# Optimization experiments

Measured on AMD Instinct MI355X. Metric: run time of the kernel, lower is better.

The kernel has to match this reference:

```python
import jax, jax.numpy as jnp
import numpy as np

T, B, OBS, LS, H, NA = 256, 1024, 128, 128, 128, 18


def setup_inputs() -> dict:
    key = jax.random.key(0)
    ks = jax.random.split(key, 20)
    rn = lambda i, shape, sc: jax.random.normal(ks[i], shape, dtype=jnp.float32) * sc
    return {
        "x": jax.random.normal(ks[0], (T * B, OBS), dtype=jnp.float32),
        "done": (jax.random.uniform(ks[1], (T * B,)) < 0.05).astype(jnp.float32),
        "h0": rn(2, (1, B, H), 0.1),
        "c0": rn(3, (1, B, H), 0.1),
        # MLP encoder: obs -> 128 -> 32 -> lstm_size
        "W1": rn(4, (128, OBS), 0.1), "b1": jnp.zeros((128,), jnp.float32),
        "W2": rn(5, (32, 128), 0.1), "b2": jnp.zeros((32,), jnp.float32),
        "W3": rn(6, (LS, 32), 0.1), "b3": jnp.zeros((LS,), jnp.float32),
        # LSTM params, PyTorch gate order [i, f, g, o]
        "Wih": rn(7, (4 * H, LS), 0.1), "Whh": rn(8, (4 * H, H), 0.1),
        "bih": jnp.zeros((4 * H,), jnp.float32), "bhh": jnp.zeros((4 * H,), jnp.float32),
        "Wa": rn(9, (NA, H), 0.01), "ba": jnp.zeros((NA,), jnp.float32),
        "Wc": rn(10, (1, H), 0.1), "bc": jnp.zeros((1,), jnp.float32),
    }


def reference(x, done, h0, c0, W1, b1, W2, b2, W3, b3, Wih, Whh, bih, bhh, Wa, ba, Wc, bc):
    # MLP encoder (self.network)
    hid = jax.nn.relu(x @ W1.T + b1)
    hid = jax.nn.relu(hid @ W2.T + b2)
    hid = jax.nn.relu(hid @ W3.T + b3)           # [T*B, LS]
    Bsz = h0.shape[1]
    hid = hid.reshape(-1, Bsz, hid.shape[-1])    # [T, B, LS]
    d = done.reshape(-1, Bsz)                    # [T, B]

    Hh = h0.shape[-1]

    def step(carry, inp):
        h, c = carry
        xt, dt = inp
        m = (1.0 - dt)[:, None]                  # reset mask
        h = h * m
        c = c * m
        gates = xt @ Wih.T + bih + h @ Whh.T + bhh   # [B, 4H]
        i = jax.nn.sigmoid(gates[:, :Hh])
        f = jax.nn.sigmoid(gates[:, Hh:2 * Hh])
        g = jnp.tanh(gates[:, 2 * Hh:3 * Hh])
        o = jax.nn.sigmoid(gates[:, 3 * Hh:])
        c = f * c + i * g
        h = o * jnp.tanh(c)
        return (h, c), h

    (hN, cN), hs = jax.lax.scan(step, (h0[0], c0[0]), (hid, d))
    flat = hs.reshape(-1, Hh)                    # [T*B, H]
    logits = flat @ Wa.T + ba                    # actor head
    value = flat @ Wc.T + bc                     # critic head
    return jnp.concatenate([logits, value], axis=-1)  # [T*B, NA+1]
```

## Files before the change

kernel.cpp:

```cpp
#include <hip/hip_runtime.h>
#include <hip/hip_bf16.h>

typedef unsigned short u16;
typedef unsigned int u32;
typedef __attribute__((ext_vector_type(8))) short short8;
typedef __attribute__((ext_vector_type(4))) float f4;
typedef __attribute__((ext_vector_type(4))) u32 u4;

#define MFMA(a, b, c) __builtin_amdgcn_mfma_f32_16x16x32_bf16((a), (b), (c), 0, 0, 0)

#define TT 256
#define BB 1024
#define NN (TT * BB)
#define NCHUNK (NN / 16)
#define WS_HID3 0
#define WS_WF   (NN * 128)
#define OFF_W1  0
#define OFF_W2  16384
#define OFF_W3  20480
#define OFF_WIH 24576
#define OFF_WHH 90112
#define OFF_WA  155648
#define WF_TOT  159744

static __device__ __forceinline__ u16 f2bf(float f) {
    u32 u = __float_as_uint(f);
    u32 r = (u + 0x7FFFu + ((u >> 16) & 1u)) >> 16;
    return (u16)r;
}
static __device__ __forceinline__ short8 pack8(f4 a, f4 b) {
    short8 r;
    r[0] = (short)f2bf(a[0]); r[1] = (short)f2bf(a[1]);
    r[2] = (short)f2bf(a[2]); r[3] = (short)f2bf(a[3]);
    r[4] = (short)f2bf(b[0]); r[5] = (short)f2bf(b[1]);
    r[6] = (short)f2bf(b[2]); r[7] = (short)f2bf(b[3]);
    return r;
}
static __device__ __forceinline__ short8 u4_to_s8(u4 v) {
    union { u4 u; short8 s; } t; t.u = v; return t.s;
}
static __device__ __forceinline__ float sigf(float x) {
    return __builtin_amdgcn_rcpf(1.f + __builtin_amdgcn_exp2f(-1.442695040888963f * x));
}
static __device__ __forceinline__ float tanhf_fast(float x) {
    return 2.f * __builtin_amdgcn_rcpf(1.f + __builtin_amdgcn_exp2f(-2.885390081777927f * x)) - 1.f;
}

static __device__ void convW128(const float* src, int Nn, u16* dst, int tid, int nth) {
    int tot = Nn * 128;
    for (int d = tid; d < tot; d += nth) {
        int j = d & 7, l = (d >> 3) & 63, ck = d >> 9;
        int kc = ck & 3, nt = ck >> 2;
        int n = nt * 16 + (l & 15), k = kc * 32 + ((l >> 4) << 3) + j;
        dst[d] = f2bf(src[n * 128 + k]);
    }
}
static __device__ void convW32(const float* src, int Nn, u16* dst, int tid, int nth) {
    int tot = Nn * 32;
    for (int d = tid; d < tot; d += nth) {
        int j = d & 7, l = (d >> 3) & 63, nt = d >> 9;
        int n = nt * 16 + (l & 15), k = ((l >> 4) << 3) + j;
        dst[d] = f2bf(src[n * 32 + k]);
    }
}

__global__ void k0_conv(const float* __restrict__ W1, const float* __restrict__ W2,
                        const float* __restrict__ W3, const float* __restrict__ Wih,
                        const float* __restrict__ Whh, const float* __restrict__ Wa,
                        const float* __restrict__ Wc, u16* __restrict__ wf) {
    int tid = blockIdx.x * blockDim.x + threadIdx.x;
    int nth = gridDim.x * blockDim.x;
    convW128(W1, 128, wf + OFF_W1, tid, nth);
    convW128(W2, 32, wf + OFF_W2, tid, nth);
    convW32(W3, 128, wf + OFF_W3, tid, nth);
    convW128(Wih, 512, wf + OFF_WIH, tid, nth);
    convW128(Whh, 512, wf + OFF_WHH, tid, nth);
    for (int d = tid; d < 32 * 128; d += nth) {
        int j = d & 7, l = (d >> 3) & 63, ck = d >> 9;
        int kc = ck & 3, nt = ck >> 2;
        int n = nt * 16 + (l & 15), k = kc * 32 + ((l >> 4) << 3) + j;
        float v = (n < 18) ? Wa[n * 128 + k] : ((n == 18) ? Wc[k] : 0.f);
        wf[OFF_WA + d] = f2bf(v);
    }
}

__global__ __launch_bounds__(256) void k1_enc(
    const float* __restrict__ x, const float* __restrict__ b1, const float* __restrict__ b2,
    const float* __restrict__ b3, const u16* __restrict__ wf, u16* __restrict__ hid3f) {
    __shared__ __align__(16) u16 scr[4][2560];

    int tid = threadIdx.x, wv = tid >> 6, lane = tid & 63;
    int m = lane & 15, q = lane >> 4;
    u16* s1 = scr[wv];
    u16* s2 = scr[wv] + 2048;
    const short8* W1v = (const short8*)(wf + OFF_W1);
    const short8* W2v = (const short8*)(wf + OFF_W2);
    const short8* W3v = (const short8*)(wf + OFF_W3);
    int wid = blockIdx.x * 4 + wv;

    for (int it = 0; it < 8; ++it) {
        int c = wid + it * 2048;
        short8 a1[4];
        const float* xr = x + (size_t)(c * 16 + m) * 128 + q * 8;
#pragma unroll
        for (int kc = 0; kc < 4; ++kc) {
            f4 f0 = *(const f4*)(xr + kc * 32);
            f4 f1 = *(const f4*)(xr + kc * 32 + 4);
            a1[kc] = pack8(f0, f1);
        }
#pragma unroll
        for (int nt = 0; nt < 8; ++nt) {
            f4 acc = {0.f, 0.f, 0.f, 0.f};
#pragma unroll
            for (int kc = 0; kc < 4; ++kc) acc = MFMA(a1[kc], W1v[(nt * 4 + kc) * 64 + lane], acc);
            int col = nt * 16 + m;
            float bb = b1[col];
            int base = (col >> 5) * 512 + ((col >> 3) & 3) * 128 + (col & 7);
#pragma unroll
            for (int p = 0; p < 4; ++p) {
                float v = acc[p] + bb; v = v > 0.f ? v : 0.f;
                s1[base + (q * 4 + p) * 8] = f2bf(v);
            }
        }
        __syncthreads();
        short8 a2[4];
#pragma unroll
        for (int kc = 0; kc < 4; ++kc) a2[kc] = *(const short8*)(s1 + kc * 512 + lane * 8);
#pragma unroll
        for (int nt = 0; nt < 2; ++nt) {
            f4 acc = {0.f, 0.f, 0.f, 0.f};
#pragma unroll
            for (int kc = 0; kc < 4; ++kc) acc = MFMA(a2[kc], W2v[(nt * 4 + kc) * 64 + lane], acc);
            int col = nt * 16 + m;
            float bb = b2[col];
            int base = (col >> 3) * 128 + (col & 7);
#pragma unroll
            for (int p = 0; p < 4; ++p) {
                float v = acc[p] + bb; v = v > 0.f ? v : 0.f;
                s2[base + (q * 4 + p) * 8] = f2bf(v);
            }
        }
        __syncthreads();
        short8 a3 = *(const short8*)(s2 + lane * 8);
#pragma unroll
        for (int nt = 0; nt < 8; ++nt) {
            f4 acc = {0.f, 0.f, 0.f, 0.f};
            acc = MFMA(a3, W3v[nt * 64 + lane], acc);
            int col = nt * 16 + m;
            float bb = b3[col];
            int base = (col >> 5) * 512 + ((col >> 3) & 3) * 128 + (col & 7);
#pragma unroll
            for (int p = 0; p < 4; ++p) {
                float v = acc[p] + bb; v = v > 0.f ? v : 0.f;
                s1[base + (q * 4 + p) * 8] = f2bf(v);
            }
        }
        __syncthreads();
        u4* dst = (u4*)hid3f + (size_t)c * 256;
#pragma unroll
        for (int kc = 0; kc < 4; ++kc) dst[kc * 64 + lane] = *(const u4*)(s1 + kc * 512 + lane * 8);
    }
}

__global__ __launch_bounds__(512) void k3_lstm(
    u16* __restrict__ hws,
    const u16* __restrict__ wf, const float* __restrict__ bih, const float* __restrict__ bhh,
    const float* __restrict__ done, const float* __restrict__ h0, const float* __restrict__ c0) {
    __shared__ __align__(16) u16 hbuf[2][2048];
    __shared__ __align__(16) float dls[4096];

    int tid = threadIdx.x, wv = tid >> 6, lane = tid & 63;
    int u15 = lane & 15, q = lane >> 4;
    int u = wv * 16 + u15;
    int rb = blockIdx.x * 16;
    const short8* WHv = (const short8*)(wf + OFF_WHH);
    const short8* WIv = (const short8*)(wf + OFF_WIH);

    short8 wh[4][4], wi[4][4];
#pragma unroll
    for (int g = 0; g < 4; ++g)
#pragma unroll
        for (int kc = 0; kc < 4; ++kc) {
            int nt = g * 8 + wv;
            wh[g][kc] = WHv[(nt * 4 + kc) * 64 + lane];
            wi[g][kc] = WIv[(nt * 4 + kc) * 64 + lane];
        }
    float bg[4];
#pragma unroll
    for (int g = 0; g < 4; ++g) bg[g] = bih[g * 128 + u] + bhh[g * 128 + u];

    for (int i = tid; i < 4096; i += 512) {
        int t = i >> 4, r = i & 15;
        dls[i] = 1.0f - done[(size_t)t * BB + rb + r];
    }
    float cst[4];
#pragma unroll
    for (int k = 0; k < 4; ++k) {
        int r = 4 * q + k;
        cst[k] = c0[(size_t)(rb + r) * 128 + u];
        float hv = h0[(size_t)(rb + r) * 128 + u];
        hbuf[0][(u >> 5) * 512 + (((u >> 3) & 3) * 16 + r) * 8 + (u & 7)] = f2bf(hv);
    }
    const u4* h3 = (const u4*)hws;
    u4 xf[4];
#pragma unroll
    for (int kc = 0; kc < 4; ++kc)
        xf[kc] = h3[((size_t)blockIdx.x * 4 + kc) * 64 + lane];
    __syncthreads();

    for (int t = 0; t < TT; ++t) {
        const u16* hc = hbuf[t & 1];
        u16* hn = hbuf[(t + 1) & 1];
        short8 ah[4];
#pragma unroll
        for (int kc = 0; kc < 4; ++kc) ah[kc] = *(const short8*)(hc + kc * 512 + lane * 8);
        f4 aH[4], aX[4];
#pragma unroll
        for (int g = 0; g < 4; ++g) { aH[g] = (f4){0.f, 0.f, 0.f, 0.f}; aX[g] = (f4){0.f, 0.f, 0.f, 0.f}; }
#pragma unroll
        for (int kc = 0; kc < 4; ++kc) {
            short8 xs = u4_to_s8(xf[kc]);
#pragma unroll
            for (int g = 0; g < 4; ++g) {
                aH[g] = MFMA(ah[kc], wh[g][kc], aH[g]);
                aX[g] = MFMA(xs, wi[g][kc], aX[g]);
            }
        }
        if (t < TT - 1) {
#pragma unroll
            for (int kc = 0; kc < 4; ++kc)
                xf[kc] = h3[(((size_t)(t + 1) * 64 + blockIdx.x) * 4 + kc) * 64 + lane];
        }
        f4 dm = *(const f4*)(dls + t * 16 + 4 * q);
#pragma unroll
        for (int k = 0; k < 4; ++k) {
            float mm = dm[k];
            float ip = aX[0][k] + bg[0] + mm * aH[0][k];
            float fp = aX[1][k] + bg[1] + mm * aH[1][k];
            float gp = aX[2][k] + bg[2] + mm * aH[2][k];
            float op = aX[3][k] + bg[3] + mm * aH[3][k];
            float ii = sigf(ip), ff = sigf(fp), gg = tanhf_fast(gp), oo = sigf(op);
            float cc = ff * (mm * cst[k]) + ii * gg;
            cst[k] = cc;
            float hh = oo * tanhf_fast(cc);
            hn[(u >> 5) * 512 + (((u >> 3) & 3) * 16 + (4 * q + k)) * 8 + (u & 7)] = f2bf(hh);
        }
        __syncthreads();
        if (wv < 4) {
            u4 v = *(const u4*)(hn + wv * 512 + lane * 8);
            ((u4*)hws)[(((size_t)t * 64 + blockIdx.x) * 4 + wv) * 64 + lane] = v;
        }
    }
}

__global__ __launch_bounds__(256) void k4_heads(
    const u16* __restrict__ hsf, const u16* __restrict__ wf,
    const float* __restrict__ ba, const float* __restrict__ bc, float* __restrict__ out) {
    int tid = threadIdx.x, wv = tid >> 6, lane = tid & 63;
    int m = lane & 15, q = lane >> 4;
    int wid = blockIdx.x * 4 + wv;
    const short8* WAv = (const short8*)(wf + OFF_WA);
    short8 wab[2][4];
#pragma unroll
    for (int nt = 0; nt < 2; ++nt)
#pragma unroll
        for (int kc = 0; kc < 4; ++kc) wab[nt][kc] = WAv[(nt * 4 + kc) * 64 + lane];
    const short8* A = (const short8*)hsf;
    for (int it = 0; it < 8; ++it) {
        int c = wid + it * 2048;
        short8 a[4];
#pragma unroll
        for (int kc = 0; kc < 4; ++kc) a[kc] = A[((size_t)c * 4 + kc) * 64 + lane];
#pragma unroll
        for (int nt = 0; nt < 2; ++nt) {
            f4 acc = {0.f, 0.f, 0.f, 0.f};
#pragma unroll
            for (int kc = 0; kc < 4; ++kc) acc = MFMA(a[kc], wab[nt][kc], acc);
            int col = nt * 16 + m;
            if (col < 19) {
                float bb = (col < 18) ? ba[col] : bc[0];
#pragma unroll
                for (int p = 0; p < 4; ++p)
                    out[(size_t)(c * 16 + q * 4 + p) * 19 + col] = acc[p] + bb;
            }
        }
    }
}

extern "C" void kernel_launch(void* const* d_in, const int* in_sizes, int n_in,
                              void* d_out, int out_size, void* d_ws, size_t ws_size,
                              hipStream_t stream) {
    const float* x    = (const float*)d_in[0];
    const float* done = (const float*)d_in[1];
    const float* h0   = (const float*)d_in[2];
    const float* c0   = (const float*)d_in[3];
    const float* W1   = (const float*)d_in[4];
    const float* b1   = (const float*)d_in[5];
    const float* W2   = (const float*)d_in[6];
    const float* b2   = (const float*)d_in[7];
    const float* W3   = (const float*)d_in[8];
    const float* b3   = (const float*)d_in[9];
    const float* Wih  = (const float*)d_in[10];
    const float* Whh  = (const float*)d_in[11];
    const float* bih  = (const float*)d_in[12];
    const float* bhh  = (const float*)d_in[13];
    const float* Wa   = (const float*)d_in[14];
    const float* ba   = (const float*)d_in[15];
    const float* Wc   = (const float*)d_in[16];
    const float* bc   = (const float*)d_in[17];
    float* out = (float*)d_out;

    u16* ws = (u16*)d_ws;
    u16* hid3f = ws + WS_HID3;
    u16* wf    = ws + WS_WF;

    hipLaunchKernelGGL(k0_conv, dim3(128), dim3(256), 0, stream,
                       W1, W2, W3, Wih, Whh, Wa, Wc, wf);
    hipLaunchKernelGGL(k1_enc, dim3(512), dim3(256), 0, stream,
                       x, b1, b2, b3, wf, hid3f);
    hipLaunchKernelGGL(k3_lstm, dim3(64), dim3(512), 0, stream,
                       hid3f, wf, bih, bhh, done, h0, c0);
    hipLaunchKernelGGL(k4_heads, dim3(512), dim3(256), 0, stream,
                       hid3f, wf, ba, bc, out);
}
```

Before: 577.0 us.

## Fuse encoder, LSTM recurrence and heads into one per-batch-slice kernel

Replaces the separate encoder, LSTM and head kernels with one 64-block kernel. Each block first encodes its own 16-row batch slice for all timesteps into a block-local workspace layout, then runs the recurrence and computes the actor/critic heads inline from the previous step's hidden state. This removes the global hs writeback, the separate heads pass and two launches, and folds the gate bias into the accumulator init. The cost is that the encoder now runs on only 64 blocks instead of 512, which serialises a large MLP workload in front of the recurrence. It also swaps some __syncthreads for raw waitcnt and s_barrier, which depend on per-wave LDS ordering being sufficient.

```diff
diff --git a/kernel.cpp b/kernel.cpp
--- a/kernel.cpp
+++ b/kernel.cpp
@@ -12,7 +12,6 @@
 #define TT 256
 #define BB 1024
 #define NN (TT * BB)
-#define NCHUNK (NN / 16)
 #define WS_HID3 0
 #define WS_WF   (NN * 128)
 #define OFF_W1  0
@@ -84,115 +83,98 @@
     }
 }
 
-__global__ __launch_bounds__(256) void k1_enc(
+__global__ __launch_bounds__(512) void k_fused(
     const float* __restrict__ x, const float* __restrict__ b1, const float* __restrict__ b2,
-    const float* __restrict__ b3, const u16* __restrict__ wf, u16* __restrict__ hid3f) {
-    __shared__ __align__(16) u16 scr[4][2560];
+    const float* __restrict__ b3, const u16* __restrict__ wf, u16* __restrict__ hid3,
+    const float* __restrict__ bih, const float* __restrict__ bhh,
+    const float* __restrict__ done, const float* __restrict__ h0, const float* __restrict__ c0,
+    const float* __restrict__ ba, const float* __restrict__ bc, float* __restrict__ out) {
+    __shared__ __align__(16) u16 smem[8 * 2560];
 
     int tid = threadIdx.x, wv = tid >> 6, lane = tid & 63;
     int m = lane & 15, q = lane >> 4;
-    u16* s1 = scr[wv];
-    u16* s2 = scr[wv] + 2048;
-    const short8* W1v = (const short8*)(wf + OFF_W1);
-    const short8* W2v = (const short8*)(wf + OFF_W2);
-    const short8* W3v = (const short8*)(wf + OFF_W3);
-    int wid = blockIdx.x * 4 + wv;
-
-    for (int it = 0; it < 8; ++it) {
-        int c = wid + it * 2048;
-        short8 a1[4];
-        const float* xr = x + (size_t)(c * 16 + m) * 128 + q * 8;
-#pragma unroll
-        for (int kc = 0; kc < 4; ++kc) {
-            f4 f0 = *(const f4*)(xr + kc * 32);
-            f4 f1 = *(const f4*)(xr + kc * 32 + 4);
-            a1[kc] = pack8(f0, f1);
-        }
-#pragma unroll
-        for (int nt = 0; nt < 8; ++nt) {
-            f4 acc = {0.f, 0.f, 0.f, 0.f};
-#pragma unroll
-            for (int kc = 0; kc < 4; ++kc) acc = MFMA(a1[kc], W1v[(nt * 4 + kc) * 64 + lane], acc);
-            int col = nt * 16 + m;
-            float bb = b1[col];
-            int base = (col >> 5) * 512 + ((col >> 3) & 3) * 128 + (col & 7);
-#pragma unroll
-            for (int p = 0; p < 4; ++p) {
-                float v = acc[p] + bb; v = v > 0.f ? v : 0.f;
-                s1[base + (q * 4 + p) * 8] = f2bf(v);
-            }
-        }
-        __syncthreads();
-        short8 a2[4];
-#pragma unroll
-        for (int kc = 0; kc < 4; ++kc) a2[kc] = *(const short8*)(s1 + kc * 512 + lane * 8);
-#pragma unroll
-        for (int nt = 0; nt < 2; ++nt) {
-            f4 acc = {0.f, 0.f, 0.f, 0.f};
-#pragma unroll
-            for (int kc = 0; kc < 4; ++kc) acc = MFMA(a2[kc], W2v[(nt * 4 + kc) * 64 + lane], acc);
-            int col = nt * 16 + m;
-            float bb = b2[col];
-            int base = (col >> 3) * 128 + (col & 7);
-#pragma unroll
-            for (int p = 0; p < 4; ++p) {
-                float v = acc[p] + bb; v = v > 0.f ? v : 0.f;
-                s2[base + (q * 4 + p) * 8] = f2bf(v);
-            }
-        }
-        __syncthreads();
-        short8 a3 = *(const short8*)(s2 + lane * 8);
-#pragma unroll
-        for (int nt = 0; nt < 8; ++nt) {
-            f4 acc = {0.f, 0.f, 0.f, 0.f};
-            acc = MFMA(a3, W3v[nt * 64 + lane], acc);
-            int col = nt * 16 + m;
-            float bb = b3[col];
-            int base = (col >> 5) * 512 + ((col >> 3) & 3) * 128 + (col & 7);
-#pragma unroll
-            for (int p = 0; p < 4; ++p) {
-                float v = acc[p] + bb; v = v > 0.f ? v : 0.f;
-                s1[base + (q * 4 + p) * 8] = f2bf(v);
-            }
-        }
-        __syncthreads();
-        u4* dst = (u4*)hid3f + (size_t)c * 256;
-#pragma unroll
-        for (int kc = 0; kc < 4; ++kc) dst[kc * 64 + lane] = *(const u4*)(s1 + kc * 512 + lane * 8);
-    }
-}
-
-__global__ __launch_bounds__(512) void k3_lstm(
-    u16* __restrict__ hws,
-    const u16* __restrict__ wf, const float* __restrict__ bih, const float* __restrict__ bhh,
-    const float* __restrict__ done, const float* __restrict__ h0, const float* __restrict__ c0) {
-    __shared__ __align__(16) u16 hbuf[2][2048];
-    __shared__ __align__(16) float dls[4096];
-
-    int tid = threadIdx.x, wv = tid >> 6, lane = tid & 63;
-    int u15 = lane & 15, q = lane >> 4;
-    int u = wv * 16 + u15;
-    int rb = blockIdx.x * 16;
-    const short8* WHv = (const short8*)(wf + OFF_WHH);
-    const short8* WIv = (const short8*)(wf + OFF_WIH);
-
-    short8 wh[4][4], wi[4][4];
-#pragma unroll
-    for (int g = 0; g < 4; ++g)
-#pragma unroll
-        for (int kc = 0; kc < 4; ++kc) {
-            int nt = g * 8 + wv;
-            wh[g][kc] = WHv[(nt * 4 + kc) * 64 + lane];
-            wi[g][kc] = WIv[(nt * 4 + kc) * 64 + lane];
-        }
-    float bg[4];
-#pragma unroll
-    for (int g = 0; g < 4; ++g) bg[g] = bih[g * 128 + u] + bhh[g * 128 + u];
-
+    int bI = blockIdx.x;
+
+    {
+        u16* s1 = smem + wv * 2560;
+        u16* s2 = s1 + 2048;
+        const short8* W1v = (const short8*)(wf + OFF_W1);
+        const short8* W2v = (const short8*)(wf + OFF_W2);
+        const short8* W3v = (const short8*)(wf + OFF_W3);
+        for (int tt = 31; tt >= 0; --tt) {
+            int t = tt * 8 + wv;
+            const float* xr = x + ((size_t)t * 1024 + bI * 16 + m) * 128 + q * 8;
+            short8 a1[4];
+#pragma unroll
+            for (int kc = 0; kc < 4; ++kc) {
+                f4 f0 = *(const f4*)(xr + kc * 32);
+                f4 f1 = *(const f4*)(xr + kc * 32 + 4);
+                a1[kc] = pack8(f0, f1);
+            }
+#pragma unroll
+            for (int nt = 0; nt < 8; ++nt) {
+                f4 acc = {0.f, 0.f, 0.f, 0.f};
+#pragma unroll
+                for (int kc = 0; kc < 4; ++kc) acc = MFMA(a1[kc], W1v[(nt * 4 + kc) * 64 + lane], acc);
+                int col = nt * 16 + m;
+                float bb = b1[col];
+                int base = (col >> 5) * 512 + ((col >> 3) & 3) * 128 + (col & 7);
+#pragma unroll
+                for (int p = 0; p < 4; ++p) {
+                    float v = acc[p] + bb; v = v > 0.f ? v : 0.f;
+                    s1[base + (q * 4 + p) * 8] = f2bf(v);
+                }
+            }
+            asm volatile("s_waitcnt lgkmcnt(0)" ::: "memory");
+            short8 a2[4];
+#pragma unroll
+            for (int kc = 0; kc < 4; ++kc) a2[kc] = *(const short8*)(s1 + kc * 512 + lane * 8);
+#pragma unroll
+            for (int nt = 0; nt < 2; ++nt) {
+                f4 acc = {0.f, 0.f, 0.f, 0.f};
+#pragma unroll
+                for (int kc = 0; kc < 4; ++kc) acc = MFMA(a2[kc], W2v[(nt * 4 + kc) * 64 + lane], acc);
+                int col = nt * 16 + m;
+                float bb = b2[col];
+                int base = (col >> 3) * 128 + (col & 7);
+#pragma unroll
+                for (int p = 0; p < 4; ++p) {
+                    float v = acc[p] + bb; v = v > 0.f ? v : 0.f;
+                    s2[base + (q * 4 + p) * 8] = f2bf(v);
+                }
+            }
+            asm volatile("s_waitcnt lgkmcnt(0)" ::: "memory");
+            short8 a3 = *(const short8*)(s2 + lane * 8);
+#pragma unroll
+            for (int nt = 0; nt < 8; ++nt) {
+                f4 acc = {0.f, 0.f, 0.f, 0.f};
+                acc = MFMA(a3, W3v[nt * 64 + lane], acc);
+                int col = nt * 16 + m;
+                float bb = b3[col];
+                int base = (col >> 5) * 512 + ((col >> 3) & 3) * 128 + (col & 7);
+#pragma unroll
+                for (int p = 0; p < 4; ++p) {
+                    float v = acc[p] + bb; v = v > 0.f ? v : 0.f;
+                    s1[base + (q * 4 + p) * 8] = f2bf(v);
+                }
+            }
+            asm volatile("s_waitcnt lgkmcnt(0)" ::: "memory");
+            u4* dst = (u4*)hid3 + ((size_t)bI * 256 + t) * 256;
+#pragma unroll
+            for (int kc = 0; kc < 4; ++kc) dst[kc * 64 + lane] = *(const u4*)(s1 + kc * 512 + lane * 8);
+        }
+    }
+    __syncthreads();
+
+    u16 (*hbuf)[2048] = (u16(*)[2048])smem;
+    float* dls = (float*)(smem + 4096);
+
+    int rb = bI * 16;
     for (int i = tid; i < 4096; i += 512) {
         int t = i >> 4, r = i & 15;
         dls[i] = 1.0f - done[(size_t)t * BB + rb + r];
     }
+    int u = wv * 16 + m;
     float cst[4];
 #pragma unroll
     for (int k = 0; k < 4; ++k) {
@@ -201,11 +183,34 @@
         float hv = h0[(size_t)(rb + r) * 128 + u];
         hbuf[0][(u >> 5) * 512 + (((u >> 3) & 3) * 16 + r) * 8 + (u & 7)] = f2bf(hv);
     }
-    const u4* h3 = (const u4*)hws;
+    const short8* WHv = (const short8*)(wf + OFF_WHH);
+    const short8* WIv = (const short8*)(wf + OFF_WIH);
+    const short8* WAv = (const short8*)(wf + OFF_WA);
+    short8 wh[4][4], wi[4][4];
+#pragma unroll
+    for (int g = 0; g < 4; ++g)
+#pragma unroll
+        for (int kc = 0; kc < 4; ++kc) {
+            int nt = g * 8 + wv;
+            wh[g][kc] = WHv[(nt * 4 + kc) * 64 + lane];
+            wi[g][kc] = WIv[(nt * 4 + kc) * 64 + lane];
+        }
+    float bg[4];
+#pragma unroll
+    for (int g = 0; g < 4; ++g) bg[g] = bih[g * 128 + u] + bhh[g * 128 + u];
+    short8 wab[4];
+    float hb = 0.f;
+    int hcol = wv * 16 + m;
+    if (wv < 2) {
+#pragma unroll
+        for (int kc = 0; kc < 4; ++kc) wab[kc] = WAv[(wv * 4 + kc) * 64 + lane];
+        if (hcol < 18) hb = ba[hcol];
+        else if (hcol == 18) hb = bc[0];
+    }
+    const u4* h3 = (const u4*)hid3 + (size_t)bI * 65536;
     u4 xf[4];
 #pragma unroll
-    for (int kc = 0; kc < 4; ++kc)
-        xf[kc] = h3[((size_t)blockIdx.x * 4 + kc) * 64 + lane];
+    for (int kc = 0; kc < 4; ++kc) xf[kc] = h3[kc * 64 + lane];
     __syncthreads();
 
     for (int t = 0; t < TT; ++t) {
@@ -216,7 +221,10 @@
         for (int kc = 0; kc < 4; ++kc) ah[kc] = *(const short8*)(hc + kc * 512 + lane * 8);
         f4 aH[4], aX[4];
 #pragma unroll
-        for (int g = 0; g < 4; ++g) { aH[g] = (f4){0.f, 0.f, 0.f, 0.f}; aX[g] = (f4){0.f, 0.f, 0.f, 0.f}; }
+        for (int g = 0; g < 4; ++g) {
+            aH[g] = (f4){0.f, 0.f, 0.f, 0.f};
+            aX[g] = (f4){bg[g], bg[g], bg[g], bg[g]};
+        }
 #pragma unroll
         for (int kc = 0; kc < 4; ++kc) {
             short8 xs = u4_to_s8(xf[kc]);
@@ -229,60 +237,47 @@
         if (t < TT - 1) {
 #pragma unroll
             for (int kc = 0; kc < 4; ++kc)
-                xf[kc] = h3[(((size_t)(t + 1) * 64 + blockIdx.x) * 4 + kc) * 64 + lane];
+                xf[kc] = h3[(size_t)(t + 1) * 256 + kc * 64 + lane];
+        }
+        if (wv < 2 && t > 0) {
+            f4 hacc = {0.f, 0.f, 0.f, 0.f};
+#pragma unroll
+            for (int kc = 0; kc < 4; ++kc) hacc = MFMA(ah[kc], wab[kc], hacc);
+            if (hcol < 19) {
+                size_t n0 = (size_t)(t - 1) * 1024 + rb + 4 * q;
+#pragma unroll
+                for (int p = 0; p < 4; ++p) out[(n0 + p) * 19 + hcol] = hacc[p] + hb;
+            }
         }
         f4 dm = *(const f4*)(dls + t * 16 + 4 * q);
 #pragma unroll
         for (int k = 0; k < 4; ++k) {
             float mm = dm[k];
-            float ip = aX[0][k] + bg[0] + mm * aH[0][k];
-            float fp = aX[1][k] + bg[1] + mm * aH[1][k];
-            float gp = aX[2][k] + bg[2] + mm * aH[2][k];
-            float op = aX[3][k] + bg[3] + mm * aH[3][k];
+            float ip = aX[0][k] + mm * aH[0][k];
+            float fp = aX[1][k] + mm * aH[1][k];
+            float gp = aX[2][k] + mm * aH[2][k];
+            float op = aX[3][k] + mm * aH[3][k];
             float ii = sigf(ip), ff = sigf(fp), gg = tanhf_fast(gp), oo = sigf(op);
             float cc = ff * (mm * cst[k]) + ii * gg;
             cst[k] = cc;
             float hh = oo * tanhf_fast(cc);
             hn[(u >> 5) * 512 + (((u >> 3) & 3) * 16 + (4 * q + k)) * 8 + (u & 7)] = f2bf(hh);
         }
-        __syncthreads();
-        if (wv < 4) {
-            u4 v = *(const u4*)(hn + wv * 512 + lane * 8);
-            ((u4*)hws)[(((size_t)t * 64 + blockIdx.x) * 4 + wv) * 64 + lane] = v;
-        }
-    }
-}
-
-__global__ __launch_bounds__(256) void k4_heads(
-    const u16* __restrict__ hsf, const u16* __restrict__ wf,
-    const float* __restrict__ ba, const float* __restrict__ bc, float* __restrict__ out) {
-    int tid = threadIdx.x, wv = tid >> 6, lane = tid & 63;
-    int m = lane & 15, q = lane >> 4;
-    int wid = blockIdx.x * 4 + wv;
-    const short8* WAv = (const short8*)(wf + OFF_WA);
-    short8 wab[2][4];
-#pragma unroll
-    for (int nt = 0; nt < 2; ++nt)
-#pragma unroll
-        for (int kc = 0; kc < 4; ++kc) wab[nt][kc] = WAv[(nt * 4 + kc) * 64 + lane];
-    const short8* A = (const short8*)hsf;
-    for (int it = 0; it < 8; ++it) {
-        int c = wid + it * 2048;
-        short8 a[4];
-#pragma unroll
-        for (int kc = 0; kc < 4; ++kc) a[kc] = A[((size_t)c * 4 + kc) * 64 + lane];
-#pragma unroll
-        for (int nt = 0; nt < 2; ++nt) {
-            f4 acc = {0.f, 0.f, 0.f, 0.f};
-#pragma unroll
-            for (int kc = 0; kc < 4; ++kc) acc = MFMA(a[kc], wab[nt][kc], acc);
-            int col = nt * 16 + m;
-            if (col < 19) {
-                float bb = (col < 18) ? ba[col] : bc[0];
-#pragma unroll
-                for (int p = 0; p < 4; ++p)
-                    out[(size_t)(c * 16 + q * 4 + p) * 19 + col] = acc[p] + bb;
-            }
+        asm volatile("s_waitcnt lgkmcnt(0)" ::: "memory");
+        __builtin_amdgcn_s_barrier();
+        asm volatile("" ::: "memory");
+    }
+    if (wv < 2) {
+        short8 ah[4];
+#pragma unroll
+        for (int kc = 0; kc < 4; ++kc) ah[kc] = *(const short8*)(hbuf[0] + kc * 512 + lane * 8);
+        f4 hacc = {0.f, 0.f, 0.f, 0.f};
+#pragma unroll
+        for (int kc = 0; kc < 4; ++kc) hacc = MFMA(ah[kc], wab[kc], hacc);
+        if (hcol < 19) {
+            size_t n0 = (size_t)255 * 1024 + rb + 4 * q;
+#pragma unroll
+            for (int p = 0; p < 4; ++p) out[(n0 + p) * 19 + hcol] = hacc[p] + hb;
         }
     }
 }
@@ -316,10 +311,6 @@
 
     hipLaunchKernelGGL(k0_conv, dim3(128), dim3(256), 0, stream,
                        W1, W2, W3, Wih, Whh, Wa, Wc, wf);
-    hipLaunchKernelGGL(k1_enc, dim3(512), dim3(256), 0, stream,
-                       x, b1, b2, b3, wf, hid3f);
-    hipLaunchKernelGGL(k3_lstm, dim3(64), dim3(512), 0, stream,
-                       hid3f, wf, bih, bhh, done, h0, c0);
-    hipLaunchKernelGGL(k4_heads, dim3(512), dim3(256), 0, stream,
-                       hid3f, wf, ba, bc, out);
-}
+    hipLaunchKernelGGL(k_fused, dim3(64), dim3(512), 0, stream,
+                       x, b1, b2, b3, wf, hid3f, bih, bhh, done, h0, c0, ba, bc, out);
+}
```

New measurement: 667.0 us. 1.16x slower.
